# Optimization experiments

Hardware: AMD Instinct MI355X
Metric: run time of the kernel (lower is better)

Reference implementation:

```python
import jax, jax.numpy as jnp
import numpy as np

TEMP = 8.0      # config.router_temp
TOP_K = 2       # config.moe_top_k
EPS = 1e-8
LN_EPS = 1e-5


def _layer_norm_noaffine(x):
    # nn.LayerNorm(input_dim, elementwise_affine=False)
    mu = jnp.mean(x, axis=-1, keepdims=True)
    var = jnp.var(x, axis=-1, keepdims=True)
    return (x - mu) / jnp.sqrt(var + LN_EPS)


def _unit_norm(x):
    # x / x.norm(dim=-1).clamp(min=EPS)
    n = jnp.linalg.norm(x, axis=-1, keepdims=True)
    return x / jnp.maximum(n, EPS)


def setup_inputs() -> dict:
    key = jax.random.key(0)
    k1, k2 = jax.random.split(key)
    x = jax.random.normal(k1, (4, 4096, 2048), dtype=jnp.float32)
    prototypes = jax.random.normal(k2, (64, 2048), dtype=jnp.float32)
    return {"x": x, "prototypes": prototypes}


def reference(x, prototypes):
    # input_norm_fn = 'norm_d', proto_norm_fn = 'unit'
    xn = _layer_norm_noaffine(x)          # [b, s, d]
    pn = _unit_norm(prototypes)           # [e, d]
    logits = jnp.einsum('bsd,ed->bse', xn, pn) / TEMP   # [b, s, e]
    probs = jax.nn.softmax(logits, axis=-1)
    top_w, top_i = jax.lax.top_k(probs, TOP_K)          # [b, s, k]
    top_w = top_w / jnp.sum(top_w, axis=-1, keepdims=True)
    return top_w, top_i
```

## Files before the change

kernel.cpp:

```cpp
#include <hip/hip_runtime.h>
#include <math.h>

typedef __attribute__((ext_vector_type(8)))  short short8;
typedef __attribute__((ext_vector_type(16))) float f32x16;

constexpr int kD  = 2048;
constexpr int kE  = 64;
constexpr int kM  = 64;
constexpr int kBK = 64;
constexpr int kIt = kD / kBK;

constexpr int kXBuf = 64 * 256;

constexpr int kPlaneU = 2 * 64 * 2 * 64 * 8;
__device__ unsigned short g_B[3 * kPlaneU];

#define GLOAD_LDS16(gp, lp)                                                   \
  __builtin_amdgcn_global_load_lds(                                          \
      (const __attribute__((address_space(1))) unsigned int*)(gp),           \
      (__attribute__((address_space(3))) unsigned int*)(lp), 16, 0, 0)

__device__ __forceinline__ void split3(float v, unsigned& h, unsigned& m, unsigned& l) {
  unsigned u = __float_as_uint(v);
  h = u & 0xFFFF0000u;
  float r1 = v - __uint_as_float(h);
  m = __float_as_uint(r1) & 0xFFFF0000u;
  float r2 = r1 - __uint_as_float(m);
  l = __float_as_uint(r2);
}

__device__ __forceinline__ void pack2(float e0, float e1,
                                      unsigned& dh, unsigned& dm, unsigned& dl) {
  unsigned h0, m0, l0, h1, m1, l1;
  split3(e0, h0, m0, l0);
  split3(e1, h1, m1, l1);
  dh = (h0 >> 16) | h1;
  dm = (m0 >> 16) | m1;
  dl = (l0 >> 16) | (l1 & 0xFFFF0000u);
}

__device__ __forceinline__ void mk_frag(float4 va, float4 vb,
                                        short8& Ah, short8& Am, short8& Al) {
  unsigned h0,m0,l0,h1,m1,l1,h2,m2,l2,h3,m3,l3;
  pack2(va.x, va.y, h0, m0, l0);
  pack2(va.z, va.w, h1, m1, l1);
  pack2(vb.x, vb.y, h2, m2, l2);
  pack2(vb.z, vb.w, h3, m3, l3);
  union { unsigned u[4]; short8 s; } U;
  U.u[0]=h0; U.u[1]=h1; U.u[2]=h2; U.u[3]=h3; Ah = U.s;
  U.u[0]=m0; U.u[1]=m1; U.u[2]=m2; U.u[3]=m3; Am = U.s;
  U.u[0]=l0; U.u[1]=l1; U.u[2]=l2; U.u[3]=l3; Al = U.s;
}

__global__ __launch_bounds__(256) void proto_prep(const float* __restrict__ p,
                                                  float* __restrict__ ws) {
  const int e = blockIdx.x, t = threadIdx.x;
  const float* row = p + (size_t)e * kD;
  float4 v0 = *(const float4*)(row + 8 * t);
  float4 v1 = *(const float4*)(row + 8 * t + 4);

  unsigned dh[4], dm[4], dl[4];
  pack2(v0.x, v0.y, dh[0], dm[0], dl[0]);
  pack2(v0.z, v0.w, dh[1], dm[1], dl[1]);
  pack2(v1.x, v1.y, dh[2], dm[2], dl[2]);
  pack2(v1.z, v1.w, dh[3], dm[3], dl[3]);
  const int gc = t >> 2;
  const int kh = (t >> 1) & 1;
  const int lb = t & 1;
  size_t base = ((((size_t)(e >> 5) * 64 + gc) * 2 + kh) * 64
                 + ((e & 31) | (lb << 5))) * 8;
  *(uint4*)&g_B[base]               = make_uint4(dh[0], dh[1], dh[2], dh[3]);
  *(uint4*)&g_B[kPlaneU + base]     = make_uint4(dm[0], dm[1], dm[2], dm[3]);
  *(uint4*)&g_B[2 * kPlaneU + base] = make_uint4(dl[0], dl[1], dl[2], dl[3]);

  float s = (v0.x + v0.y) + (v0.z + v0.w) + (v1.x + v1.y) + (v1.z + v1.w);
  float q = v0.x*v0.x + v0.y*v0.y + v0.z*v0.z + v0.w*v0.w
          + v1.x*v1.x + v1.y*v1.y + v1.z*v1.z + v1.w*v1.w;
  #pragma unroll
  for (int off = 32; off >= 1; off >>= 1) {
    s += __shfl_xor(s, off, 64);
    q += __shfl_xor(q, off, 64);
  }
  __shared__ float as[4], aq[4];
  if ((t & 63) == 0) { as[t >> 6] = s; aq[t >> 6] = q; }
  __syncthreads();
  if (t == 0) {
    float S = (as[0] + as[1]) + (as[2] + as[3]);
    float Q = (aq[0] + aq[1]) + (aq[2] + aq[3]);
    ws[e]      = S;
    ws[kE + e] = 1.f / fmaxf(sqrtf(Q), 1e-8f);
  }
}

__global__ __launch_bounds__(512, 2) void router_main(
    const float* __restrict__ x, const float* __restrict__ ws,
    float* __restrict__ out_w, float* __restrict__ out_i) {
  __shared__ __align__(16) unsigned char sA[3 * kXBuf];

  const int t    = threadIdx.x;
  const int w    = t >> 6;
  const int L    = t & 63;
  const int tt   = w >> 2;
  const int eg   = (w >> 1) & 1;
  const int kp   = w & 1;
  const int tok0 = blockIdx.x * kM;
  const float* xg = x + (size_t)tok0 * kD;

  auto stageIt = [&](int its, int bufI) {
    unsigned char* base = sA + bufI * kXBuf;
    const int kbase = its * kBK;
    #pragma unroll
    for (int qq = 0; qq < 2; ++qq) {
      const int r0  = w * 8 + qq * 4;
      const int row = r0 + (L >> 4);
      const int slot = (L & 15) ^ (row & 15);
      const float* gp = xg + (size_t)row * kD + kbase + slot * 4;
      unsigned char* lp = base + r0 * 256 + L * 16;
      GLOAD_LDS16(gp, lp);
    }
  };

  auto bIdx = [&](int g, int kh) -> size_t {
    return ((((size_t)eg * 64 + g) * 2 + kh) * 64 + L) * 8;
  };

  f32x16 accA, accB;
  #pragma unroll
  for (int i = 0; i < 16; ++i) { accA[i] = 0.f; accB[i] = 0.f; }
  float sx = 0.f, sxx = 0.f;

  stageIt(0, 0);
  stageIt(1, 1);
  short8 BcH0, BcM0, BcL0, BcH1, BcM1, BcL1;
  {
    size_t b0 = bIdx(kp, 0), b1 = bIdx(kp, 1);
    BcH0 = *(const short8*)&g_B[b0];
    BcM0 = *(const short8*)&g_B[kPlaneU + b0];
    BcL0 = *(const short8*)&g_B[2 * kPlaneU + b0];
    BcH1 = *(const short8*)&g_B[b1];
    BcM1 = *(const short8*)&g_B[kPlaneU + b1];
    BcL1 = *(const short8*)&g_B[2 * kPlaneU + b1];
  }

  const int aRow  = tt * 32 + (L & 31);
  const unsigned char* rRow0 = sA + aRow * 256;
  const int sw    = aRow & 15;
  const int sBase = kp * 8 + 2 * (L >> 5);

  for (int it = 0; it < kIt; ++it) {
    short8 BnH0 = BcH0, BnM0 = BcM0, BnL0 = BcL0;
    short8 BnH1 = BcH1, BnM1 = BcM1, BnL1 = BcL1;
    if (it + 1 < kIt) {
      const int g1 = 2 * (it + 1) + kp;
      size_t b0 = bIdx(g1, 0), b1 = bIdx(g1, 1);
      BnH0 = *(const short8*)&g_B[b0];
      BnM0 = *(const short8*)&g_B[kPlaneU + b0];
      BnL0 = *(const short8*)&g_B[2 * kPlaneU + b0];
      BnH1 = *(const short8*)&g_B[b1];
      BnM1 = *(const short8*)&g_B[kPlaneU + b1];
      BnL1 = *(const short8*)&g_B[2 * kPlaneU + b1];
    }

    if (it + 1 < kIt) asm volatile("s_waitcnt vmcnt(14)" ::: "memory");
    else              asm volatile("s_waitcnt vmcnt(6)"  ::: "memory");
    __builtin_amdgcn_sched_barrier(0);

    __builtin_amdgcn_s_barrier();
    __builtin_amdgcn_sched_barrier(0);

    if (it + 2 < kIt) stageIt(it + 2, (it + 2) % 3);

    const unsigned char* rb = rRow0 + (it % 3) * kXBuf;
    float4 va0 = *(const float4*)(rb + (((sBase    )     ) ^ sw) * 16);
    float4 vb0 = *(const float4*)(rb + (((sBase    ) + 1 ) ^ sw) * 16);
    float4 va1 = *(const float4*)(rb + (((sBase + 4)     ) ^ sw) * 16);
    float4 vb1 = *(const float4*)(rb + (((sBase + 4) + 1 ) ^ sw) * 16);

    if (eg == 0) {
      sx  += ((va0.x + va0.y) + (va0.z + va0.w)) + ((vb0.x + vb0.y) + (vb0.z + vb0.w))
           + ((va1.x + va1.y) + (va1.z + va1.w)) + ((vb1.x + vb1.y) + (vb1.z + vb1.w));
      float q0 = fmaf(va0.x,va0.x, fmaf(va0.y,va0.y, fmaf(va0.z,va0.z, va0.w*va0.w)));
      float q1 = fmaf(vb0.x,vb0.x, fmaf(vb0.y,vb0.y, fmaf(vb0.z,vb0.z, vb0.w*vb0.w)));
      float q2 = fmaf(va1.x,va1.x, fmaf(va1.y,va1.y, fmaf(va1.z,va1.z, va1.w*va1.w)));
      float q3 = fmaf(vb1.x,vb1.x, fmaf(vb1.y,vb1.y, fmaf(vb1.z,vb1.z, vb1.w*vb1.w)));
      sxx += (q0 + q1) + (q2 + q3);
    }

    short8 Ah0, Am0, Al0, Ah1, Am1, Al1;
    mk_frag(va0, vb0, Ah0, Am0, Al0);
    mk_frag(va1, vb1, Ah1, Am1, Al1);

    __builtin_amdgcn_s_setprio(1);
    accA = __builtin_amdgcn_mfma_f32_32x32x16_bf16(Ah0, BcH0, accA, 0, 0, 0);
    accB = __builtin_amdgcn_mfma_f32_32x32x16_bf16(Ah1, BcH1, accB, 0, 0, 0);
    accA = __builtin_amdgcn_mfma_f32_32x32x16_bf16(Ah0, BcM0, accA, 0, 0, 0);
    accB = __builtin_amdgcn_mfma_f32_32x32x16_bf16(Ah1, BcM1, accB, 0, 0, 0);
    accA = __builtin_amdgcn_mfma_f32_32x32x16_bf16(Am0, BcH0, accA, 0, 0, 0);
    accB = __builtin_amdgcn_mfma_f32_32x32x16_bf16(Am1, BcH1, accB, 0, 0, 0);
    accA = __builtin_amdgcn_mfma_f32_32x32x16_bf16(Am0, BcM0, accA, 0, 0, 0);
    accB = __builtin_amdgcn_mfma_f32_32x32x16_bf16(Am1, BcM1, accB, 0, 0, 0);
    accA = __builtin_amdgcn_mfma_f32_32x32x16_bf16(Ah0, BcL0, accA, 0, 0, 0);
    accB = __builtin_amdgcn_mfma_f32_32x32x16_bf16(Ah1, BcL1, accB, 0, 0, 0);
    accA = __builtin_amdgcn_mfma_f32_32x32x16_bf16(Al0, BcH0, accA, 0, 0, 0);
    accB = __builtin_amdgcn_mfma_f32_32x32x16_bf16(Al1, BcH1, accB, 0, 0, 0);
    __builtin_amdgcn_s_setprio(0);

    BcH0 = BnH0; BcM0 = BnM0; BcL0 = BnL0;
    BcH1 = BnH1; BcM1 = BnM1; BcL1 = BnL1;
  }

  __syncthreads();

  float* sLogit  = (float*)sA;
  float* sStatsP = (float*)(sA + kM * 68 * 4);

  if (eg == 0) {
    float a = sx  + __shfl_xor(sx, 32, 64);
    float b = sxx + __shfl_xor(sxx, 32, 64);
    if (L < 32) {
      int m = tt * 32 + L;
      sStatsP[(kp * kM + m) * 2 + 0] = a;
      sStatsP[(kp * kM + m) * 2 + 1] = b;
    }
  }

  if (kp == 0) {
    #pragma unroll
    for (int i = 0; i < 16; ++i) {
      int row = (i & 3) + 8 * (i >> 2) + 4 * (L >> 5);
      sLogit[(tt * 32 + row) * 68 + eg * 32 + (L & 31)] = accA[i] + accB[i];
    }
  }
  __syncthreads();
  if (kp == 1) {
    #pragma unroll
    for (int i = 0; i < 16; ++i) {
      int row = (i & 3) + 8 * (i >> 2) + 4 * (L >> 5);
      sLogit[(tt * 32 + row) * 68 + eg * 32 + (L & 31)] += accA[i] + accB[i];
    }
  }
  __syncthreads();

  const float Se  = ws[L];
  const float inv = ws[kE + L];
  #pragma unroll
  for (int tl = 0; tl < 8; ++tl) {
    int tk = w * 8 + tl;
    float st0 = sStatsP[tk * 2 + 0] + sStatsP[(kM + tk) * 2 + 0];
    float st1 = sStatsP[tk * 2 + 1] + sStatsP[(kM + tk) * 2 + 1];
    float mu   = st0 * (1.f / kD);
    float var  = st1 * (1.f / kD) - mu * mu;
    float rstd = rsqrtf(var + 1e-5f);
    float logit = (sLogit[tk * 68 + L] - mu * Se) * rstd * inv * 0.125f;

    float v1 = logit; int i1 = L;
    #pragma unroll
    for (int off = 32; off >= 1; off >>= 1) {
      float ov = __shfl_xor(v1, off, 64);
      int   oi = __shfl_xor(i1, off, 64);
      if (ov > v1 || (ov == v1 && oi < i1)) { v1 = ov; i1 = oi; }
    }
    float ml = (L == i1) ? -3.402823466e38f : logit;
    float v2 = ml; int i2 = L;
    #pragma unroll
    for (int off = 32; off >= 1; off >>= 1) {
      float ov = __shfl_xor(v2, off, 64);
      int   oi = __shfl_xor(i2, off, 64);
      if (ov > v2 || (ov == v2 && oi < i2)) { v2 = ov; i2 = oi; }
    }
    if (L == 0) {
      int tg = tok0 + tk;
      float er = expf(v2 - v1);
      float r  = 1.f / (1.f + er);
      out_w[2 * tg]     = r;
      out_w[2 * tg + 1] = er * r;
      out_i[2 * tg]     = (float)i1;
      out_i[2 * tg + 1] = (float)i2;
    }
  }
}

extern "C" void kernel_launch(void* const* d_in, const int* in_sizes, int n_in,
                              void* d_out, int out_size, void* d_ws, size_t ws_size,
                              hipStream_t stream) {
  const float* x = (const float*)d_in[0];
  const float* p = (const float*)d_in[1];
  float* ws = (float*)d_ws;
  const int T = in_sizes[0] / kD;
  float* out_w = (float*)d_out;
  float* out_i = (float*)d_out + (size_t)T * 2;

  proto_prep<<<kE, 256, 0, stream>>>(p, ws);
  router_main<<<T / kM, 512, 0, stream>>>(x, ws, out_w, out_i);
}
```

Before: 222.5 us.

## Load x fragments directly from global memory instead of LDS triple buffering

Drops the async global-to-LDS triple-buffered staging of x tiles along with its per-iteration barriers and waitcnt choreography. Each lane now reads its MFMA A fragment straight from global memory with float4 loads, and loads the B fragments in the same iteration without register prefetching. This removes barrier synchronization and most LDS use, which could allow more occupancy. The cost is that load latency is no longer hidden by explicit prefetch, and the per-lane strided row reads may coalesce less well.

```diff
diff --git a/kernel.cpp b/kernel.cpp
--- a/kernel.cpp
+++ b/kernel.cpp
@@ -7,18 +7,10 @@
 constexpr int kD  = 2048;
 constexpr int kE  = 64;
 constexpr int kM  = 64;
-constexpr int kBK = 64;
-constexpr int kIt = kD / kBK;
-
-constexpr int kXBuf = 64 * 256;
+constexpr int kIt = 32;
 
 constexpr int kPlaneU = 2 * 64 * 2 * 64 * 8;
 __device__ unsigned short g_B[3 * kPlaneU];
-
-#define GLOAD_LDS16(gp, lp)                                                   \
-  __builtin_amdgcn_global_load_lds(                                          \
-      (const __attribute__((address_space(1))) unsigned int*)(gp),           \
-      (__attribute__((address_space(3))) unsigned int*)(lp), 16, 0, 0)
 
 __device__ __forceinline__ void split3(float v, unsigned& h, unsigned& m, unsigned& l) {
   unsigned u = __float_as_uint(v);
@@ -95,7 +87,8 @@
 __global__ __launch_bounds__(512, 2) void router_main(
     const float* __restrict__ x, const float* __restrict__ ws,
     float* __restrict__ out_w, float* __restrict__ out_i) {
-  __shared__ __align__(16) unsigned char sA[3 * kXBuf];
+  __shared__ float sLogit[kM][68];
+  __shared__ float sStats[2][kM][2];
 
   const int t    = threadIdx.x;
   const int w    = t >> 6;
@@ -103,22 +96,10 @@
   const int tt   = w >> 2;
   const int eg   = (w >> 1) & 1;
   const int kp   = w & 1;
+  const int hi   = L >> 5;
+  const int row  = tt * 32 + (L & 31);
   const int tok0 = blockIdx.x * kM;
-  const float* xg = x + (size_t)tok0 * kD;
-
-  auto stageIt = [&](int its, int bufI) {
-    unsigned char* base = sA + bufI * kXBuf;
-    const int kbase = its * kBK;
-    #pragma unroll
-    for (int qq = 0; qq < 2; ++qq) {
-      const int r0  = w * 8 + qq * 4;
-      const int row = r0 + (L >> 4);
-      const int slot = (L & 15) ^ (row & 15);
-      const float* gp = xg + (size_t)row * kD + kbase + slot * 4;
-      unsigned char* lp = base + r0 * 256 + L * 16;
-      GLOAD_LDS16(gp, lp);
-    }
-  };
+  const float* xr = x + (size_t)(tok0 + row) * kD + hi * 8;
 
   auto bIdx = [&](int g, int kh) -> size_t {
     return ((((size_t)eg * 64 + g) * 2 + kh) * 64 + L) * 8;
@@ -129,52 +110,21 @@
   for (int i = 0; i < 16; ++i) { accA[i] = 0.f; accB[i] = 0.f; }
   float sx = 0.f, sxx = 0.f;
 
-  stageIt(0, 0);
-  stageIt(1, 1);
-  short8 BcH0, BcM0, BcL0, BcH1, BcM1, BcL1;
-  {
-    size_t b0 = bIdx(kp, 0), b1 = bIdx(kp, 1);
-    BcH0 = *(const short8*)&g_B[b0];
-    BcM0 = *(const short8*)&g_B[kPlaneU + b0];
-    BcL0 = *(const short8*)&g_B[2 * kPlaneU + b0];
-    BcH1 = *(const short8*)&g_B[b1];
-    BcM1 = *(const short8*)&g_B[kPlaneU + b1];
-    BcL1 = *(const short8*)&g_B[2 * kPlaneU + b1];
-  }
-
-  const int aRow  = tt * 32 + (L & 31);
-  const unsigned char* rRow0 = sA + aRow * 256;
-  const int sw    = aRow & 15;
-  const int sBase = kp * 8 + 2 * (L >> 5);
-
   for (int it = 0; it < kIt; ++it) {
-    short8 BnH0 = BcH0, BnM0 = BcM0, BnL0 = BcL0;
-    short8 BnH1 = BcH1, BnM1 = BcM1, BnL1 = BcL1;
-    if (it + 1 < kIt) {
-      const int g1 = 2 * (it + 1) + kp;
-      size_t b0 = bIdx(g1, 0), b1 = bIdx(g1, 1);
-      BnH0 = *(const short8*)&g_B[b0];
-      BnM0 = *(const short8*)&g_B[kPlaneU + b0];
-      BnL0 = *(const short8*)&g_B[2 * kPlaneU + b0];
-      BnH1 = *(const short8*)&g_B[b1];
-      BnM1 = *(const short8*)&g_B[kPlaneU + b1];
-      BnL1 = *(const short8*)&g_B[2 * kPlaneU + b1];
-    }
-
-    if (it + 1 < kIt) asm volatile("s_waitcnt vmcnt(14)" ::: "memory");
-    else              asm volatile("s_waitcnt vmcnt(6)"  ::: "memory");
-    __builtin_amdgcn_sched_barrier(0);
-
-    __builtin_amdgcn_s_barrier();
-    __builtin_amdgcn_sched_barrier(0);
-
-    if (it + 2 < kIt) stageIt(it + 2, (it + 2) % 3);
-
-    const unsigned char* rb = rRow0 + (it % 3) * kXBuf;
-    float4 va0 = *(const float4*)(rb + (((sBase    )     ) ^ sw) * 16);
-    float4 vb0 = *(const float4*)(rb + (((sBase    ) + 1 ) ^ sw) * 16);
-    float4 va1 = *(const float4*)(rb + (((sBase + 4)     ) ^ sw) * 16);
-    float4 vb1 = *(const float4*)(rb + (((sBase + 4) + 1 ) ^ sw) * 16);
+    const int g = 2 * it + kp;
+
+    float4 va0 = *(const float4*)(xr + 32 * g);
+    float4 vb0 = *(const float4*)(xr + 32 * g + 4);
+    float4 va1 = *(const float4*)(xr + 32 * g + 16);
+    float4 vb1 = *(const float4*)(xr + 32 * g + 20);
+
+    const size_t b0 = bIdx(g, 0), b1 = bIdx(g, 1);
+    short8 BH0 = *(const short8*)&g_B[b0];
+    short8 BM0 = *(const short8*)&g_B[kPlaneU + b0];
+    short8 BL0 = *(const short8*)&g_B[2 * kPlaneU + b0];
+    short8 BH1 = *(const short8*)&g_B[b1];
+    short8 BM1 = *(const short8*)&g_B[kPlaneU + b1];
+    short8 BL1 = *(const short8*)&g_B[2 * kPlaneU + b1];
 
     if (eg == 0) {
       sx  += ((va0.x + va0.y) + (va0.z + va0.w)) + ((vb0.x + vb0.y) + (vb0.z + vb0.w))
@@ -191,52 +141,44 @@
     mk_frag(va1, vb1, Ah1, Am1, Al1);
 
     __builtin_amdgcn_s_setprio(1);
-    accA = __builtin_amdgcn_mfma_f32_32x32x16_bf16(Ah0, BcH0, accA, 0, 0, 0);
-    accB = __builtin_amdgcn_mfma_f32_32x32x16_bf16(Ah1, BcH1, accB, 0, 0, 0);
-    accA = __builtin_amdgcn_mfma_f32_32x32x16_bf16(Ah0, BcM0, accA, 0, 0, 0);
-    accB = __builtin_amdgcn_mfma_f32_32x32x16_bf16(Ah1, BcM1, accB, 0, 0, 0);
-    accA = __builtin_amdgcn_mfma_f32_32x32x16_bf16(Am0, BcH0, accA, 0, 0, 0);
-    accB = __builtin_amdgcn_mfma_f32_32x32x16_bf16(Am1, BcH1, accB, 0, 0, 0);
-    accA = __builtin_amdgcn_mfma_f32_32x32x16_bf16(Am0, BcM0, accA, 0, 0, 0);
-    accB = __builtin_amdgcn_mfma_f32_32x32x16_bf16(Am1, BcM1, accB, 0, 0, 0);
-    accA = __builtin_amdgcn_mfma_f32_32x32x16_bf16(Ah0, BcL0, accA, 0, 0, 0);
-    accB = __builtin_amdgcn_mfma_f32_32x32x16_bf16(Ah1, BcL1, accB, 0, 0, 0);
-    accA = __builtin_amdgcn_mfma_f32_32x32x16_bf16(Al0, BcH0, accA, 0, 0, 0);
-    accB = __builtin_amdgcn_mfma_f32_32x32x16_bf16(Al1, BcH1, accB, 0, 0, 0);
+    accA = __builtin_amdgcn_mfma_f32_32x32x16_bf16(Ah0, BH0, accA, 0, 0, 0);
+    accB = __builtin_amdgcn_mfma_f32_32x32x16_bf16(Ah1, BH1, accB, 0, 0, 0);
+    accA = __builtin_amdgcn_mfma_f32_32x32x16_bf16(Ah0, BM0, accA, 0, 0, 0);
+    accB = __builtin_amdgcn_mfma_f32_32x32x16_bf16(Ah1, BM1, accB, 0, 0, 0);
+    accA = __builtin_amdgcn_mfma_f32_32x32x16_bf16(Am0, BH0, accA, 0, 0, 0);
+    accB = __builtin_amdgcn_mfma_f32_32x32x16_bf16(Am1, BH1, accB, 0, 0, 0);
+    accA = __builtin_amdgcn_mfma_f32_32x32x16_bf16(Am0, BM0, accA, 0, 0, 0);
+    accB = __builtin_amdgcn_mfma_f32_32x32x16_bf16(Am1, BM1, accB, 0, 0, 0);
+    accA = __builtin_amdgcn_mfma_f32_32x32x16_bf16(Ah0, BL0, accA, 0, 0, 0);
+    accB = __builtin_amdgcn_mfma_f32_32x32x16_bf16(Ah1, BL1, accB, 0, 0, 0);
+    accA = __builtin_amdgcn_mfma_f32_32x32x16_bf16(Al0, BH0, accA, 0, 0, 0);
+    accB = __builtin_amdgcn_mfma_f32_32x32x16_bf16(Al1, BH1, accB, 0, 0, 0);
     __builtin_amdgcn_s_setprio(0);
-
-    BcH0 = BnH0; BcM0 = BnM0; BcL0 = BnL0;
-    BcH1 = BnH1; BcM1 = BnM1; BcL1 = BnL1;
-  }
-
-  __syncthreads();
-
-  float* sLogit  = (float*)sA;
-  float* sStatsP = (float*)(sA + kM * 68 * 4);
+  }
 
   if (eg == 0) {
     float a = sx  + __shfl_xor(sx, 32, 64);
     float b = sxx + __shfl_xor(sxx, 32, 64);
     if (L < 32) {
       int m = tt * 32 + L;
-      sStatsP[(kp * kM + m) * 2 + 0] = a;
-      sStatsP[(kp * kM + m) * 2 + 1] = b;
+      sStats[kp][m][0] = a;
+      sStats[kp][m][1] = b;
     }
   }
 
   if (kp == 0) {
     #pragma unroll
     for (int i = 0; i < 16; ++i) {
-      int row = (i & 3) + 8 * (i >> 2) + 4 * (L >> 5);
-      sLogit[(tt * 32 + row) * 68 + eg * 32 + (L & 31)] = accA[i] + accB[i];
+      int r = (i & 3) + 8 * (i >> 2) + 4 * hi;
+      sLogit[tt * 32 + r][eg * 32 + (L & 31)] = accA[i] + accB[i];
     }
   }
   __syncthreads();
   if (kp == 1) {
     #pragma unroll
     for (int i = 0; i < 16; ++i) {
-      int row = (i & 3) + 8 * (i >> 2) + 4 * (L >> 5);
-      sLogit[(tt * 32 + row) * 68 + eg * 32 + (L & 31)] += accA[i] + accB[i];
+      int r = (i & 3) + 8 * (i >> 2) + 4 * hi;
+      sLogit[tt * 32 + r][eg * 32 + (L & 31)] += accA[i] + accB[i];
     }
   }
   __syncthreads();
@@ -246,12 +188,12 @@
   #pragma unroll
   for (int tl = 0; tl < 8; ++tl) {
     int tk = w * 8 + tl;
-    float st0 = sStatsP[tk * 2 + 0] + sStatsP[(kM + tk) * 2 + 0];
-    float st1 = sStatsP[tk * 2 + 1] + sStatsP[(kM + tk) * 2 + 1];
+    float st0 = sStats[0][tk][0] + sStats[1][tk][0];
+    float st1 = sStats[0][tk][1] + sStats[1][tk][1];
     float mu   = st0 * (1.f / kD);
     float var  = st1 * (1.f / kD) - mu * mu;
     float rstd = rsqrtf(var + 1e-5f);
-    float logit = (sLogit[tk * 68 + L] - mu * Se) * rstd * inv * 0.125f;
+    float logit = (sLogit[tk][L] - mu * Se) * rstd * inv * 0.125f;
 
     float v1 = logit; int i1 = L;
     #pragma unroll
```

Result: no change. 224.4 us (+0.9%).
